# Optimization experiments

Hardware: AMD Instinct MI355X
Metric: run time of the kernel (lower is better)

The kernel has to match this reference:

```python
import jax, jax.numpy as jnp
import numpy as np

DIM = 1024
NUM_HEADS = 16
HEAD_D = DIM // NUM_HEADS


def setup_inputs() -> dict:
    key = jax.random.key(0)
    ks = jax.random.split(key, 9)
    s = 1.0 / np.sqrt(DIM)
    x = jax.random.normal(ks[0], (2, 2048, DIM), dtype=jnp.float32)
    Wq = jax.random.uniform(ks[1], (DIM, DIM), jnp.float32, -s, s)
    bq = jax.random.uniform(ks[2], (DIM,), jnp.float32, -s, s)
    Wk = jax.random.uniform(ks[3], (DIM, DIM), jnp.float32, -s, s)
    bk = jax.random.uniform(ks[4], (DIM,), jnp.float32, -s, s)
    Wv = jax.random.uniform(ks[5], (DIM, DIM), jnp.float32, -s, s)
    bv = jax.random.uniform(ks[6], (DIM,), jnp.float32, -s, s)
    Wo = jax.random.uniform(ks[7], (DIM, DIM), jnp.float32, -s, s)
    bo = jax.random.uniform(ks[8], (DIM,), jnp.float32, -s, s)
    return {"x": x, "Wq": Wq, "bq": bq, "Wk": Wk, "bk": bk,
            "Wv": Wv, "bv": bv, "Wo": Wo, "bo": bo}


def reference(x, Wq, bq, Wk, bk, Wv, bv, Wo, bo):
    B, T, D = x.shape
    H, Hd = NUM_HEADS, HEAD_D
    # torch Linear: x @ W.T + b
    q = (x @ Wq.T + bq).reshape(B, T, H, Hd).transpose(0, 2, 1, 3)  # [B,H,T,Hd]
    k = (x @ Wk.T + bk).reshape(B, T, H, Hd).transpose(0, 2, 1, 3)
    v = (x @ Wv.T + bv).reshape(B, T, H, Hd).transpose(0, 2, 1, 3)
    scores = jnp.einsum('bhqd,bhkd->bhqk', q, k) / jnp.sqrt(jnp.float32(Hd))
    causal = jnp.tril(jnp.ones((T, T), dtype=bool))  # [T,T]
    scores = jnp.where(causal[None, None], scores, -jnp.inf)
    probs = jax.nn.softmax(scores, axis=-1)
    ctx = jnp.einsum('bhqk,bhkd->bhqd', probs, v)
    out = ctx.transpose(0, 2, 1, 3).reshape(B, T, D)
    out = out @ Wo.T + bo
    return (out, (k, v))
```

## Files before the change

kernel.cpp:

```cpp
#include <hip/hip_runtime.h>

#define BB 2
#define TT 2048
#define DD 1024
#define HH 16
#define HD 64
#define MM (BB*TT)

typedef __bf16 bf16;
typedef __bf16 bf16x4 __attribute__((ext_vector_type(4)));
typedef __bf16 bf16x8 __attribute__((ext_vector_type(8)));
typedef float  f32x4  __attribute__((ext_vector_type(4)));

#define QSCALE 0.1803368801111244f
#define M0 16.0f

__device__ __forceinline__ void gl_lds16(const void* g, void* l) {
  __builtin_amdgcn_global_load_lds(
      (const __attribute__((address_space(1))) void*)g,
      (__attribute__((address_space(3))) void*)l, 16, 0, 0);
}
__device__ __forceinline__ f32x4 mfma16(bf16x8 a, bf16x8 b, f32x4 c) {
  return __builtin_amdgcn_mfma_f32_16x16x32_bf16(a, b, c, 0, 0, 0);
}

__global__ void cvt_all(const float* __restrict__ x,
                        const float* __restrict__ w0, const float* __restrict__ w1,
                        const float* __restrict__ w2, const float* __restrict__ w3,
                        bf16* __restrict__ xd,
                        bf16* __restrict__ d0, bf16* __restrict__ d1,
                        bf16* __restrict__ d2, bf16* __restrict__ d3) {
  int i = blockIdx.x * blockDim.x + threadIdx.x;
  const float* s;
  bf16* d;
  int off;
  if (i < (1 << 20)) { s = x; d = xd; off = i; }
  else {
    int j = (i - (1 << 20)) >> 18;
    off = (i - (1 << 20)) & ((1 << 18) - 1);
    s = (j == 0) ? w0 : (j == 1) ? w1 : (j == 2) ? w2 : w3;
    d = (j == 0) ? d0 : (j == 1) ? d1 : (j == 2) ? d2 : d3;
  }
  float4 v = ((const float4*)s)[off];
  bf16x4 o = { (bf16)v.x, (bf16)v.y, (bf16)v.z, (bf16)v.w };
  ((bf16x4*)d)[off] = o;
}

template<int BM, int BN>
__device__ __forceinline__ void tile_core64(const bf16* __restrict__ A,
                                            const bf16* __restrict__ W,
                                            int m0, int n0,
                                            bf16* sA, bf16* sB,
                                            f32x4 (&acc)[BM/32][BN/32]) {
  const int tid  = threadIdx.x;
  const int wv   = tid >> 6;
  const int l15  = tid & 15;
  const int quad = (tid & 63) >> 4;
  const int wy   = wv >> 1, wx = wv & 1;
  const int MI_  = BM / 32, NI_ = BN / 32;
  const int srow = tid >> 3;
  const int schk = (tid & 7) ^ (srow & 7);
  const int rswz = l15 & 7;
  const bf16* Ab = A + (size_t)(m0 + srow) * DD + schk * 8;
  const bf16* Wb = W + (size_t)(n0 + srow) * DD + schk * 8;
  char* lA = (char*)sA + wv * 1024;
  char* lB = (char*)sB + wv * 1024;
  for (int k0 = 0; k0 < DD; k0 += 64) {
#pragma unroll
    for (int j = 0; j < BM / 32; j++)
      gl_lds16(Ab + (size_t)j * 32 * DD + k0, lA + j * 4096);
#pragma unroll
    for (int j = 0; j < BN / 32; j++)
      gl_lds16(Wb + (size_t)j * 32 * DD + k0, lB + j * 4096);
    __syncthreads();
#pragma unroll
    for (int h = 0; h < 2; h++) {
      bf16x8 af[MI_], bw[NI_];
#pragma unroll
      for (int mi = 0; mi < MI_; mi++)
        af[mi] = *(const bf16x8*)(sA + (wy * (BM / 2) + mi * 16 + l15) * 64
                                     + (((h * 4 + quad) ^ rswz) * 8));
#pragma unroll
      for (int ni = 0; ni < NI_; ni++)
        bw[ni] = *(const bf16x8*)(sB + (wx * (BN / 2) + ni * 16 + l15) * 64
                                     + (((h * 4 + quad) ^ rswz) * 8));
#pragma unroll
      for (int mi = 0; mi < MI_; mi++)
#pragma unroll
        for (int ni = 0; ni < NI_; ni++)
          acc[mi][ni] = mfma16(af[mi], bw[ni], acc[mi][ni]);
    }
    __syncthreads();
  }
}

__launch_bounds__(256)
__global__ void gemm_qkv(const bf16* __restrict__ X,
                         const bf16* __restrict__ Wq, const bf16* __restrict__ Wk,
                         const bf16* __restrict__ Wv,
                         const float* __restrict__ bq, const float* __restrict__ bk,
                         const float* __restrict__ bv,
                         bf16* __restrict__ qb, bf16* __restrict__ kb,
                         bf16* __restrict__ vtb,
                         float* __restrict__ kf, float* __restrict__ vf) {
  __shared__ bf16 sA[128 * 64];
  __shared__ bf16 sB[128 * 64];
  const int bid = blockIdx.x;
  const int wv_ = threadIdx.x >> 6;
  const int l15 = threadIdx.x & 15, quad = (threadIdx.x & 63) >> 4;
  const int wy = wv_ >> 1, wx = wv_ & 1;
  if (bid < 512) {
    const int sel = bid >> 8;
    const bf16*  W    = sel ? Wk : Wq;
    const float* bias = sel ? bk : bq;
    const int m0 = ((bid & 255) >> 3) * 128;
    const int n0 = (bid & 7) * 128;
    f32x4 acc[4][4] = {};
    tile_core64<128, 128>(X, W, m0, n0, sA, sB, acc);
    for (int mi = 0; mi < 4; mi++)
      for (int ni = 0; ni < 4; ni++)
        for (int r = 0; r < 4; r++) {
          int m = m0 + wy * 64 + mi * 16 + quad * 4 + r;
          int n = n0 + wx * 64 + ni * 16 + l15;
          float v = acc[mi][ni][r] + bias[n];
          int b = m >> 11, t = m & (TT - 1);
          int h = n >> 6,  d = n & (HD - 1);
          size_t idx = ((size_t)(b * HH + h) * TT + t) * HD + d;
          if (sel == 0) qb[idx] = (bf16)(v * QSCALE);
          else { kb[idx] = (bf16)v; kf[idx] = v; }
        }
  } else {
    const int sub = bid - 512;
    const int m0 = (sub >> 5) * 128;
    const int n0 = (sub & 31) * 128;
    f32x4 acc[4][4] = {};
    tile_core64<128, 128>(Wv, X, m0, n0, sA, sB, acc);
    for (int mi = 0; mi < 4; mi++) {
      int mbase = m0 + wy * 64 + mi * 16 + quad * 4;
      float brv[4];
      for (int r = 0; r < 4; r++) brv[r] = bv[mbase + r];
      int h = mbase >> 6, dbase = mbase & (HD - 1);
      for (int ni = 0; ni < 4; ni++) {
        int tok = n0 + wx * 64 + ni * 16 + l15;
        int b = tok >> 11, t = tok & (TT - 1);
        int bh = b * HH + h;
        float4 vv;
        float* vp = &vv.x;
        for (int r = 0; r < 4; r++) {
          float v = acc[mi][ni][r] + brv[r];
          vp[r] = v;
          vtb[((size_t)bh * HD + dbase + r) * TT + t] = (bf16)v;
        }
        *(float4*)&vf[((size_t)bh * TT + t) * HD + dbase] = vv;
      }
    }
  }
}

__launch_bounds__(256)
__global__ void gemm_o(const bf16* __restrict__ A, const bf16* __restrict__ W,
                       const float* __restrict__ bias, float* __restrict__ out) {
  __shared__ bf16 sA[64 * 64];
  __shared__ bf16 sB[128 * 64];
  const int m0 = blockIdx.x * 64;
  const int n0 = blockIdx.y * 128;
  f32x4 acc[2][4] = {};
  tile_core64<64, 128>(A, W, m0, n0, sA, sB, acc);
  const int wv = threadIdx.x >> 6;
  const int l15 = threadIdx.x & 15, quad = (threadIdx.x & 63) >> 4;
  const int wy = wv >> 1, wx = wv & 1;
  for (int mi = 0; mi < 2; mi++)
    for (int ni = 0; ni < 4; ni++)
      for (int r = 0; r < 4; r++) {
        int m = m0 + wy * 32 + mi * 16 + quad * 4 + r;
        int n = n0 + wx * 64 + ni * 16 + l15;
        out[(size_t)m * DD + n] = acc[mi][ni][r] + bias[n];
      }
}

__launch_bounds__(256, 4)
__global__ void attn_fwd(const bf16* __restrict__ Q, const bf16* __restrict__ Kg,
                         const bf16* __restrict__ Vt, bf16* __restrict__ ctx) {
  __shared__ __align__(16) bf16 kbuf[2][4096];
  __shared__ __align__(16) bf16 vbuf[2][4096];
  __shared__ __align__(16) bf16 pbuf[4][1024];
  const int tid  = threadIdx.x;
  const int lane = tid & 63, wv = tid >> 6;
  const int quad = lane >> 4, l15 = lane & 15;
  const int bx = blockIdx.x;
  const int sl = bx >> 3;
  const int c  = 31 - (sl >> 2);
  const int bh = (bx & 7) + 8 * (sl & 3);
  const int qr = c * 64 + wv * 16;
  const int ntiles = c + 1;

  const bf16* Kbh = Kg + (size_t)bh * TT * HD;
  const bf16* Vbh = Vt + (size_t)bh * HD * TT;

  const int k0s = tid >> 3,  c0s = (tid & 7) ^ (k0s & 7);
  const int s1  = 256 + tid;
  const int k1s = s1 >> 3,   c1s = (s1 & 7) ^ (k1s & 7);

  int foff[4][2];
  for (int sub = 0; sub < 4; sub++)
    for (int h = 0; h < 2; h++)
      foff[sub][h] = (((sub * 16 + l15) * 8) + ((h * 4 + quad) ^ (l15 & 7))) * 8;

  const bf16* qp = Q + ((size_t)bh * TT + qr + l15) * HD + quad * 8;
  bf16x8 aq0 = *(const bf16x8*)qp;
  bf16x8 aq1 = *(const bf16x8*)(qp + 32);

  float lrow = 0.f;
  f32x4 acc[4] = {};
  bf16* pb = pbuf[wv];
  const int pswz = l15 & 7;

  gl_lds16(Kbh + (size_t)k0s * HD + c0s * 8, (char*)kbuf[0] + wv * 1024);
  gl_lds16(Kbh + (size_t)k1s * HD + c1s * 8, (char*)kbuf[0] + 4096 + wv * 1024);
  gl_lds16(Vbh + (size_t)k0s * TT + c0s * 8, (char*)vbuf[0] + wv * 1024);
  gl_lds16(Vbh + (size_t)k1s * TT + c1s * 8, (char*)vbuf[0] + 4096 + wv * 1024);

  for (int t = 0; t < ntiles; t++) {
    const int kt = t * 64;
    __syncthreads();
    if (t + 1 < ntiles) {
      bf16* kn = kbuf[(t + 1) & 1];
      bf16* vn = vbuf[(t + 1) & 1];
      gl_lds16(Kbh + (size_t)(kt + 64 + k0s) * HD + c0s * 8, (char*)kn + wv * 1024);
      gl_lds16(Kbh + (size_t)(kt + 64 + k1s) * HD + c1s * 8, (char*)kn + 4096 + wv * 1024);
      gl_lds16(Vbh + (size_t)k0s * TT + kt + 64 + c0s * 8, (char*)vn + wv * 1024);
      gl_lds16(Vbh + (size_t)k1s * TT + kt + 64 + c1s * 8, (char*)vn + 4096 + wv * 1024);
    }
    const bf16* kc = kbuf[t & 1];
    const bf16* vc = vbuf[t & 1];
    const bool last = (t == ntiles - 1);

    float p[4][4];
    for (int sub = 0; sub < 4; sub++) {
      if (last && kt + sub * 16 > qr + 15) {
        p[sub][0] = p[sub][1] = p[sub][2] = p[sub][3] = 0.f;
        continue;
      }
      bf16x8 ak0 = *(const bf16x8*)(kc + foff[sub][0]);
      bf16x8 ak1 = *(const bf16x8*)(kc + foff[sub][1]);
      f32x4 z = {};
      f32x4 st = mfma16(ak0, aq0, z);
      st = mfma16(ak1, aq1, st);
      if (last) {
        for (int r = 0; r < 4; r++) {
          int k_abs = kt + sub * 16 + quad * 4 + r;
          p[sub][r] = (k_abs > qr + l15) ? 0.f
                      : __builtin_amdgcn_exp2f(st[r] - M0);
        }
      } else {
        for (int r = 0; r < 4; r++)
          p[sub][r] = __builtin_amdgcn_exp2f(st[r] - M0);
      }
      lrow += (p[sub][0] + p[sub][1]) + (p[sub][2] + p[sub][3]);
    }

    for (int sub = 0; sub < 4; sub++) {
      bf16x4 pk = { (bf16)p[sub][0], (bf16)p[sub][1], (bf16)p[sub][2], (bf16)p[sub][3] };
      int cch = sub * 2 + (quad >> 1);
      *(bf16x4*)&pb[l15 * 64 + ((cch ^ pswz) * 8 + (quad & 1) * 4)] = pk;
    }
    bf16x8 ap0 = *(const bf16x8*)&pb[l15 * 64 + ((quad ^ pswz) * 8)];
    bf16x8 ap1 = *(const bf16x8*)&pb[l15 * 64 + (((4 + quad) ^ pswz) * 8)];

    for (int ni = 0; ni < 4; ni++) {
      bf16x8 v0 = *(const bf16x8*)(vc + foff[ni][0]);
      bf16x8 v1 = *(const bf16x8*)(vc + foff[ni][1]);
      acc[ni] = mfma16(ap0, v0, acc[ni]);
      acc[ni] = mfma16(ap1, v1, acc[ni]);
    }
  }

  lrow += __shfl_xor(lrow, 16, 64);
  lrow += __shfl_xor(lrow, 32, 64);
  float invl = 1.f / lrow;
  float invq[4];
  for (int r = 0; r < 4; r++)
    invq[r] = __shfl(invl, (lane & 48) | (quad * 4 + r), 64);
  int b = bh >> 4, h = bh & (HH - 1);
  for (int ni = 0; ni < 4; ni++)
    for (int r = 0; r < 4; r++) {
      int tq = qr + quad * 4 + r;
      ctx[((size_t)(b * TT + tq)) * DD + h * HD + ni * 16 + l15] = (bf16)(acc[ni][r] * invq[r]);
    }
}

extern "C" void kernel_launch(void* const* d_in, const int* in_sizes, int n_in,
                              void* d_out, int out_size, void* d_ws, size_t ws_size,
                              hipStream_t stream) {
  const float* x  = (const float*)d_in[0];
  const float* Wq = (const float*)d_in[1];
  const float* bq = (const float*)d_in[2];
  const float* Wk = (const float*)d_in[3];
  const float* bk = (const float*)d_in[4];
  const float* Wv = (const float*)d_in[5];
  const float* bv = (const float*)d_in[6];
  const float* Wo = (const float*)d_in[7];
  const float* bo = (const float*)d_in[8];
  float* out = (float*)d_out;
  float* outK = out + (size_t)MM * DD;
  float* outV = out + (size_t)2 * MM * DD;

  char* ws = (char*)d_ws;
  bf16* xb   = (bf16*)(ws);
  bf16* wqb  = (bf16*)(ws + (8  << 20));
  bf16* wkb  = (bf16*)(ws + (10 << 20));
  bf16* wvb  = (bf16*)(ws + (12 << 20));
  bf16* wob  = (bf16*)(ws + (14 << 20));
  bf16* qbuf = (bf16*)(ws + (16 << 20));
  bf16* kbuf = (bf16*)(ws + (24 << 20));
  bf16* vtb  = (bf16*)(ws + (32 << 20));
  bf16* ctxb = (bf16*)(ws + (40 << 20));

  cvt_all<<<(2 << 20) / 256, 256, 0, stream>>>(x, Wq, Wk, Wv, Wo,
                                               xb, wqb, wkb, wvb, wob);

  gemm_qkv<<<768, 256, 0, stream>>>(xb, wqb, wkb, wvb, bq, bk, bv,
                                    qbuf, kbuf, vtb, outK, outV);

  attn_fwd<<<1024, 256, 0, stream>>>(qbuf, kbuf, vtb, ctxb);

  gemm_o<<<dim3(MM / 64, DD / 128), 256, 0, stream>>>(ctxb, wob, bo, out);
}
```

Before: 190.0 us.

## Fuse Q and K projections sharing X tile in 512-thread QKV GEMM

Rewrites the QKV projection kernel so one block computes both the Q and K tiles for the same X rows. The X tile is loaded into shared memory once per k-step and reused for both weight matrices. Blocks grow to 512 threads (8 waves) with a 32-wide K step, and the V blocks are interleaved with the Q/K blocks, giving a 512-block grid. In exchange the shared-memory tiles lose their XOR swizzle, which may cause LDS bank conflicts. Each k-step also does less MFMA work per barrier, so sync overhead rises.

```diff
diff --git a/kernel.cpp b/kernel.cpp
--- a/kernel.cpp
+++ b/kernel.cpp
@@ -46,6 +46,119 @@
   ((bf16x4*)d)[off] = o;
 }
 
+__launch_bounds__(512)
+__global__ void gemm_qkv(const bf16* __restrict__ X,
+                         const bf16* __restrict__ Wq, const bf16* __restrict__ Wk,
+                         const bf16* __restrict__ Wv,
+                         const float* __restrict__ bq, const float* __restrict__ bk,
+                         const float* __restrict__ bv,
+                         bf16* __restrict__ qb, bf16* __restrict__ kb,
+                         bf16* __restrict__ vtb,
+                         float* __restrict__ kf, float* __restrict__ vf) {
+  __shared__ bf16 sA[128 * 32];
+  __shared__ bf16 sB[2][128 * 32];
+  const int tid  = threadIdx.x;
+  const int wv   = tid >> 6;
+  const int lane = tid & 63;
+  const int quad = lane >> 4, l15 = lane & 15;
+  const int wy   = wv >> 1, wx = wv & 1;
+  const int g    = blockIdx.x >> 4;
+  const int j    = blockIdx.x & 15;
+  const int row  = tid >> 2;
+  const int c8   = (tid & 3) * 8;
+  char* lA  = (char*)sA    + wv * 1024;
+  char* lB0 = (char*)sB[0] + wv * 1024;
+  char* lB1 = (char*)sB[1] + wv * 1024;
+
+  if (j < 8) {
+    const int m0 = g * 128;
+    const int n0 = j * 128;
+    const bf16* Ab  = X  + (size_t)(m0 + row) * DD + c8;
+    const bf16* Bqb = Wq + (size_t)(n0 + row) * DD + c8;
+    const bf16* Bkb = Wk + (size_t)(n0 + row) * DD + c8;
+    f32x4 accq[2][4] = {}, acck[2][4] = {};
+    for (int k0 = 0; k0 < DD; k0 += 32) {
+      gl_lds16(Ab  + k0, lA);
+      gl_lds16(Bqb + k0, lB0);
+      gl_lds16(Bkb + k0, lB1);
+      __syncthreads();
+      bf16x8 af[2], bq_[4], bk_[4];
+#pragma unroll
+      for (int mi = 0; mi < 2; mi++)
+        af[mi] = *(const bf16x8*)(sA + (wy * 32 + mi * 16 + l15) * 32 + quad * 8);
+#pragma unroll
+      for (int ni = 0; ni < 4; ni++) {
+        bq_[ni] = *(const bf16x8*)(sB[0] + (wx * 64 + ni * 16 + l15) * 32 + quad * 8);
+        bk_[ni] = *(const bf16x8*)(sB[1] + (wx * 64 + ni * 16 + l15) * 32 + quad * 8);
+      }
+#pragma unroll
+      for (int mi = 0; mi < 2; mi++)
+#pragma unroll
+        for (int ni = 0; ni < 4; ni++) {
+          accq[mi][ni] = mfma16(af[mi], bq_[ni], accq[mi][ni]);
+          acck[mi][ni] = mfma16(af[mi], bk_[ni], acck[mi][ni]);
+        }
+      __syncthreads();
+    }
+    for (int mi = 0; mi < 2; mi++)
+      for (int ni = 0; ni < 4; ni++)
+        for (int r = 0; r < 4; r++) {
+          int m = m0 + wy * 32 + mi * 16 + quad * 4 + r;
+          int n = n0 + wx * 64 + ni * 16 + l15;
+          int b = m >> 11, t = m & (TT - 1);
+          int h = n >> 6,  d = n & (HD - 1);
+          size_t idx = ((size_t)(b * HH + h) * TT + t) * HD + d;
+          qb[idx] = (bf16)((accq[mi][ni][r] + bq[n]) * QSCALE);
+          float vk = acck[mi][ni][r] + bk[n];
+          kb[idx] = (bf16)vk;
+          kf[idx] = vk;
+        }
+  } else {
+    const int m0 = (j - 8) * 128;
+    const int n0 = g * 128;
+    const bf16* Ab = Wv + (size_t)(m0 + row) * DD + c8;
+    const bf16* Bb = X  + (size_t)(n0 + row) * DD + c8;
+    f32x4 acc[2][4] = {};
+    for (int k0 = 0; k0 < DD; k0 += 32) {
+      gl_lds16(Ab + k0, lA);
+      gl_lds16(Bb + k0, lB0);
+      __syncthreads();
+      bf16x8 af[2], bx_[4];
+#pragma unroll
+      for (int mi = 0; mi < 2; mi++)
+        af[mi] = *(const bf16x8*)(sA + (wy * 32 + mi * 16 + l15) * 32 + quad * 8);
+#pragma unroll
+      for (int ni = 0; ni < 4; ni++)
+        bx_[ni] = *(const bf16x8*)(sB[0] + (wx * 64 + ni * 16 + l15) * 32 + quad * 8);
+#pragma unroll
+      for (int mi = 0; mi < 2; mi++)
+#pragma unroll
+        for (int ni = 0; ni < 4; ni++)
+          acc[mi][ni] = mfma16(af[mi], bx_[ni], acc[mi][ni]);
+      __syncthreads();
+    }
+    for (int mi = 0; mi < 2; mi++) {
+      int mbase = m0 + wy * 32 + mi * 16 + quad * 4;
+      float brv[4];
+      for (int r = 0; r < 4; r++) brv[r] = bv[mbase + r];
+      int h = mbase >> 6, dbase = mbase & (HD - 1);
+      for (int ni = 0; ni < 4; ni++) {
+        int tok = n0 + wx * 64 + ni * 16 + l15;
+        int b = tok >> 11, t = tok & (TT - 1);
+        int bh = b * HH + h;
+        float4 vv;
+        float* vp = &vv.x;
+        for (int r = 0; r < 4; r++) {
+          float v = acc[mi][ni][r] + brv[r];
+          vp[r] = v;
+          vtb[((size_t)bh * HD + dbase + r) * TT + t] = (bf16)v;
+        }
+        *(float4*)&vf[((size_t)bh * TT + t) * HD + dbase] = vv;
+      }
+    }
+  }
+}
+
 template<int BM, int BN>
 __device__ __forceinline__ void tile_core64(const bf16* __restrict__ A,
                                             const bf16* __restrict__ W,
@@ -95,69 +208,6 @@
 }
 
 __launch_bounds__(256)
-__global__ void gemm_qkv(const bf16* __restrict__ X,
-                         const bf16* __restrict__ Wq, const bf16* __restrict__ Wk,
-                         const bf16* __restrict__ Wv,
-                         const float* __restrict__ bq, const float* __restrict__ bk,
-                         const float* __restrict__ bv,
-                         bf16* __restrict__ qb, bf16* __restrict__ kb,
-                         bf16* __restrict__ vtb,
-                         float* __restrict__ kf, float* __restrict__ vf) {
-  __shared__ bf16 sA[128 * 64];
-  __shared__ bf16 sB[128 * 64];
-  const int bid = blockIdx.x;
-  const int wv_ = threadIdx.x >> 6;
-  const int l15 = threadIdx.x & 15, quad = (threadIdx.x & 63) >> 4;
-  const int wy = wv_ >> 1, wx = wv_ & 1;
-  if (bid < 512) {
-    const int sel = bid >> 8;
-    const bf16*  W    = sel ? Wk : Wq;
-    const float* bias = sel ? bk : bq;
-    const int m0 = ((bid & 255) >> 3) * 128;
-    const int n0 = (bid & 7) * 128;
-    f32x4 acc[4][4] = {};
-    tile_core64<128, 128>(X, W, m0, n0, sA, sB, acc);
-    for (int mi = 0; mi < 4; mi++)
-      for (int ni = 0; ni < 4; ni++)
-        for (int r = 0; r < 4; r++) {
-          int m = m0 + wy * 64 + mi * 16 + quad * 4 + r;
-          int n = n0 + wx * 64 + ni * 16 + l15;
-          float v = acc[mi][ni][r] + bias[n];
-          int b = m >> 11, t = m & (TT - 1);
-          int h = n >> 6,  d = n & (HD - 1);
-          size_t idx = ((size_t)(b * HH + h) * TT + t) * HD + d;
-          if (sel == 0) qb[idx] = (bf16)(v * QSCALE);
-          else { kb[idx] = (bf16)v; kf[idx] = v; }
-        }
-  } else {
-    const int sub = bid - 512;
-    const int m0 = (sub >> 5) * 128;
-    const int n0 = (sub & 31) * 128;
-    f32x4 acc[4][4] = {};
-    tile_core64<128, 128>(Wv, X, m0, n0, sA, sB, acc);
-    for (int mi = 0; mi < 4; mi++) {
-      int mbase = m0 + wy * 64 + mi * 16 + quad * 4;
-      float brv[4];
-      for (int r = 0; r < 4; r++) brv[r] = bv[mbase + r];
-      int h = mbase >> 6, dbase = mbase & (HD - 1);
-      for (int ni = 0; ni < 4; ni++) {
-        int tok = n0 + wx * 64 + ni * 16 + l15;
-        int b = tok >> 11, t = tok & (TT - 1);
-        int bh = b * HH + h;
-        float4 vv;
-        float* vp = &vv.x;
-        for (int r = 0; r < 4; r++) {
-          float v = acc[mi][ni][r] + brv[r];
-          vp[r] = v;
-          vtb[((size_t)bh * HD + dbase + r) * TT + t] = (bf16)v;
-        }
-        *(float4*)&vf[((size_t)bh * TT + t) * HD + dbase] = vv;
-      }
-    }
-  }
-}
-
-__launch_bounds__(256)
 __global__ void gemm_o(const bf16* __restrict__ A, const bf16* __restrict__ W,
                        const float* __restrict__ bias, float* __restrict__ out) {
   __shared__ bf16 sA[64 * 64];
@@ -319,7 +369,7 @@
   cvt_all<<<(2 << 20) / 256, 256, 0, stream>>>(x, Wq, Wk, Wv, Wo,
                                                xb, wqb, wkb, wvb, wob);
 
-  gemm_qkv<<<768, 256, 0, stream>>>(xb, wqb, wkb, wvb, bq, bk, bv,
+  gemm_qkv<<<512, 512, 0, stream>>>(xb, wqb, wkb, wvb, bq, bk, bv,
                                     qbuf, kbuf, vtb, outK, outV);
 
   attn_fwd<<<1024, 256, 0, stream>>>(qbuf, kbuf, vtb, ctxb);
```

After: 184.2 us. -3.0%, faster.
